# Performance work log

Measured on AMD Instinct MI355X. Metric: run time of the kernel, lower is better.

Reference implementation:

```python
import jax, jax.numpy as jnp
import numpy as np

B, C, D4, K, TOPK = 2, 16, 48, 24, 2
H, W = 512, 960
H4, W4 = H // 4, W // 4


def setup_inputs() -> dict:
    key = jax.random.key(0)
    ks = jax.random.split(key, 5)
    return {
        "att_weights": jax.random.normal(ks[0], (B, 1, D4, H4, W4), jnp.float32),
        "feat_l": jax.random.normal(ks[1], (B, C, H4, W4), jnp.float32),
        "feat_r": jax.random.normal(ks[2], (B, C, H4, W4), jnp.float32),
        "w_red": jax.random.normal(ks[3], (2 * C,), jnp.float32) / np.sqrt(2 * C).astype(np.float32),
        "spx_logits": jax.random.normal(ks[4], (B, 9, H, W), jnp.float32),
    }


def _unfold3x3(x):
    # x: [B,1,h,w] -> [B,9,h,w]; 3x3 zero-padded neighborhoods, row-major (torch F.unfold order)
    b, _, h, w = x.shape
    xp = jnp.pad(x, ((0, 0), (0, 0), (1, 1), (1, 1)))
    return jnp.concatenate([xp[:, :, dy:dy + h, dx:dx + w] for dy in range(3) for dx in range(3)], axis=1)


def _context_upsample(disp_low, spx_prob):
    # disp_low: [B,1,h,w]; spx_prob: [B,9,4h,4w] (already softmaxed over the 9 dim)
    neigh = _unfold3x3(disp_low)                                   # [B,9,h,w]
    neigh = jnp.repeat(jnp.repeat(neigh, 4, axis=2), 4, axis=3)
    return jnp.sum(neigh * spx_prob, axis=1)                        # [B,4h,4w]


def reference(att_weights, feat_l, feat_r, w_red, spx_logits):
    # ---- coarse top-K disparity selection: softmax -> sort -> gather ----
    prob = jax.nn.softmax(att_weights, axis=2)                      # [B,1,D,h,w]
    prob_t = jnp.moveaxis(prob, 2, -1)                              # [B,1,h,w,D]
    _, idx = jax.lax.top_k(prob_t, K)                               # descending by prob
    ind_k = jnp.sort(idx, axis=-1)                                  # ascending disparity order [B,1,h,w,K]
    att_topk = jnp.take_along_axis(prob_t, ind_k, axis=-1)          # [B,1,h,w,K]
    raw_t = jnp.moveaxis(att_weights, 2, -1)
    att_raw_topk = jnp.take_along_axis(raw_t, ind_k, axis=-1)       # [B,1,h,w,K]
    disp_samples = ind_k[:, 0].astype(att_weights.dtype)            # [B,h,w,K]

    att_prob = jax.nn.softmax(att_raw_topk[:, 0], axis=-1)          # [B,h,w,K]
    pred_att_x4 = jnp.sum(att_prob * disp_samples, axis=-1)         # [B,h,w]

    # ---- sparse concat volume at the K sampled disparities ----
    dK = jnp.moveaxis(ind_k[:, 0], -1, 1)                           # [B,K,h,w] int
    src = jnp.arange(W4)[None, None, None, :] - dK                  # x - d, [B,K,h,w]
    valid = (src >= 0).astype(feat_r.dtype)
    srcc = jnp.clip(src, 0, W4 - 1)
    warped_r = jnp.take_along_axis(feat_r[:, :, None, :, :], srcc[:, None], axis=-1)  # [B,C,K,h,w]
    warped_r = warped_r * valid[:, None]
    left_b = jnp.broadcast_to(feat_l[:, :, None], (feat_l.shape[0], C, K, H4, W4))
    vol = jnp.concatenate([left_b, warped_r], axis=1)               # [B,2C,K,h,w]
    vol = vol * jnp.moveaxis(att_topk, -1, 2)                       # att-weighted sparse volume

    # channel reduction -> 1-channel cost (stand-in for cat aggregation/hourglass)
    cost = jnp.einsum('bckhw,c->bkhw', vol, w_red)                  # [B,K,h,w]

    cost_t = jnp.moveaxis(cost, 1, -1)                              # [B,h,w,K]
    vals, ind2 = jax.lax.top_k(cost_t, TOPK)
    p = jax.nn.softmax(vals, axis=-1)
    dsel = jnp.take_along_axis(disp_samples, ind2, axis=-1)
    pred_x4 = jnp.sum(p * dsel, axis=-1)                            # [B,h,w]

    spx_prob = jax.nn.softmax(spx_logits, axis=1)                   # [B,9,H,W]
    pred_att_x1 = _context_upsample(pred_att_x4[:, None], spx_prob) * 4.0
    pred_x1 = _context_upsample(pred_x4[:, None], spx_prob) * 4.0
    return pred_att_x4, pred_att_x1, pred_x4, pred_x1
```

## Files before the change

### kernel.cpp

```cpp
#include <hip/hip_runtime.h>
#include <hip/hip_bf16.h>
#include <math.h>

#define Bc 2
#define Cc 16
#define D4c 48
#define Kc 24
#define Hc 512
#define Wc 960
#define H4c 128
#define W4c 240
#define HW4 (H4c * W4c)
#define S4 (Bc * HW4)
#define HW1 (Hc * Wc)
#define S1 (Bc * HW1)
#define Gg 8
#define DPT 6

__global__ __launch_bounds__(256) void k_featred(const float* __restrict__ fl,
                          const float* __restrict__ fr,
                          const float* __restrict__ wred,
                          float* __restrict__ Lred, float* __restrict__ Rred) {
    int t = blockIdx.x * blockDim.x + threadIdx.x;
    if (t >= S4 / 4) return;
    int p4 = t * 4;
    int b  = p4 / HW4;
    int hw = p4 - b * HW4;
    const float* flb = fl + (size_t)b * Cc * HW4 + hw;
    const float* frb = fr + (size_t)b * Cc * HW4 + hw;
    float4 ls = {0.f, 0.f, 0.f, 0.f}, rs = {0.f, 0.f, 0.f, 0.f};
#pragma unroll
    for (int c = 0; c < Cc; ++c) {
        float wl = wred[c], wr = wred[Cc + c];
        float4 l = *(const float4*)(flb + (size_t)c * HW4);
        float4 r = *(const float4*)(frb + (size_t)c * HW4);
        ls.x = fmaf(wl, l.x, ls.x); ls.y = fmaf(wl, l.y, ls.y);
        ls.z = fmaf(wl, l.z, ls.z); ls.w = fmaf(wl, l.w, ls.w);
        rs.x = fmaf(wr, r.x, rs.x); rs.y = fmaf(wr, r.y, rs.y);
        rs.z = fmaf(wr, r.z, rs.z); rs.w = fmaf(wr, r.w, rs.w);
    }
    *(float4*)(Lred + p4) = ls;
    *(float4*)(Rred + p4) = rs;
}

__global__ __launch_bounds__(256, 6) void k_topk(const float* __restrict__ att,
                       const float* __restrict__ Lred, const float* __restrict__ Rred,
                       float* __restrict__ oA4, float* __restrict__ oD4) {
    const int tid  = threadIdx.x;
    const int wv   = tid >> 6;
    const int lane = tid & 63;
    const int q    = lane >> 3;
    const int p    = lane & 7;
    const int pix  = blockIdx.x * 32 + wv * 8 + p;
    const int b    = pix / HW4;
    const int hw   = pix - b * HW4;
    const int col  = hw % W4c;
    const int dbase = q * DPT;

    const float* ap = att + ((size_t)b * D4c + dbase) * HW4 + hw;
    float a[DPT], RR[DPT];
#pragma unroll
    for (int i = 0; i < DPT; ++i) a[i] = ap[(size_t)i * HW4];
#pragma unroll
    for (int i = 0; i < DPT; ++i) {
        int d = dbase + i;
        RR[i] = Rred[(col >= d) ? (pix - d) : pix];
    }
    const float L = Lred[pix];

    unsigned u[DPT];
#pragma unroll
    for (int i = 0; i < DPT; ++i) {
        unsigned r = __float_as_uint(a[i]);
        u[i] = ((int)r < 0) ? ~r : (r | 0x80000000u);
    }

    float m = a[0];
#pragma unroll
    for (int i = 1; i < DPT; ++i) m = fmaxf(m, a[i]);
    m = fmaxf(m, __shfl_xor(m, 8));
    m = fmaxf(m, __shfl_xor(m, 16));
    m = fmaxf(m, __shfl_xor(m, 32));

    int bc[DPT];
#pragma unroll
    for (int i = 0; i < DPT; ++i) bc[i] = 0;
#pragma unroll
    for (int i = 0; i < DPT; ++i) {
#pragma unroll
        for (int j = i + 1; j < DPT; ++j) {
            int c = (u[i] >= u[j]) ? 1 : 0;
            bc[j] += c;
            bc[i] += 1 - c;
        }
    }
#pragma unroll 2
    for (int c = 1; c < Gg; ++c) {
        const unsigned adj = ((q ^ c) < q) ? 1u : 0u;
        unsigned ui2[DPT], uj[DPT];
#pragma unroll
        for (int i = 0; i < DPT; ++i) ui2[i] = u[i] - adj;
#pragma unroll
        for (int j = 0; j < DPT; ++j) uj[j] = __shfl_xor(u[j], c << 3);
#pragma unroll
        for (int i = 0; i < DPT; ++i) {
#pragma unroll
            for (int j = 0; j < DPT; ++j) bc[i] += (uj[j] > ui2[i]) ? 1 : 0;
        }
    }

    const float NEG = -3.0e38f;
    float s = 0.f, s2 = 0.f, n2 = 0.f;
    float v1 = NEG, v2 = NEG;
    int   i1 = 0,   i2v = 0;
#pragma unroll
    for (int i = 0; i < DPT; ++i) {
        const int d = dbase + i;
        float e = __expf(a[i] - m);
        s += e;
        bool sel = bc[i] < Kc;
        float es = sel ? e : 0.f;
        s2 += es;
        n2 = fmaf(es, (float)d, n2);
        float R = (col >= d) ? RR[i] : 0.f;
        float cst = sel ? e * (L + R) : NEG;
        bool g1 = cst > v1;
        bool g2 = cst > v2;
        float nv2 = g1 ? v1 : (g2 ? cst : v2);
        int   ni2 = g1 ? i1 : (g2 ? d : i2v);
        v1 = g1 ? cst : v1;
        i1 = g1 ? d : i1;
        v2 = nv2;
        i2v = ni2;
    }

#pragma unroll
    for (int st = 8; st <= 32; st <<= 1) {
        s  += __shfl_xor(s,  st);
        s2 += __shfl_xor(s2, st);
        n2 += __shfl_xor(n2, st);
        float ov1 = __shfl_xor(v1, st); int oi1 = __shfl_xor(i1,  st);
        float ov2 = __shfl_xor(v2, st); int oi2 = __shfl_xor(i2v, st);
        bool bt = (ov1 > v1) || (ov1 == v1 && oi1 < i1);
        float w1 = bt ? ov1 : v1;   int wi1 = bt ? oi1 : i1;
        float l1 = bt ? v1  : ov1;  int li1 = bt ? i1  : oi1;
        float w2 = bt ? ov2 : v2;   int wi2 = bt ? oi2 : i2v;
        bool b2 = (l1 > w2) || (l1 == w2 && li1 < wi2);
        v1 = w1; i1 = wi1;
        v2 = b2 ? l1 : w2;
        i2v = b2 ? li1 : wi2;
    }

    const float r = __expf((v2 - v1) / s);
    if (q == 0) {
        oA4[pix] = n2 / s2;
        oD4[pix] = ((float)i1 + r * (float)i2v) / (1.f + r);
    }
}

__global__ __launch_bounds__(256) void k_upsample(const float* __restrict__ spx,
                           const float* __restrict__ A4, const float* __restrict__ D4p,
                           float* __restrict__ oA1, float* __restrict__ oD1) {
    int t = blockIdx.x * blockDim.x + threadIdx.x;
    if (t >= S1 / 4) return;
    const int Wq  = Wc / 4;
    int xg  = t % Wq;
    int rem = t / Wq;
    int y   = rem % Hc;
    int b   = rem / Hc;
    int yx0 = y * Wc + xg * 4;

    const float* sp = spx + (size_t)b * 9 * HW1 + yx0;
    float4 e[9];
    float4 ssum = {0.f, 0.f, 0.f, 0.f};
#pragma unroll
    for (int j = 0; j < 9; ++j) {
        float4 v = *(const float4*)(sp + (size_t)j * HW1);
        e[j].x = __expf(v.x); e[j].y = __expf(v.y);
        e[j].z = __expf(v.z); e[j].w = __expf(v.w);
        ssum.x += e[j].x; ssum.y += e[j].y; ssum.z += e[j].z; ssum.w += e[j].w;
    }

    const int y4 = y >> 2, x4 = xg;
    const float* A4b = A4 + b * HW4;
    const float* D4b = D4p + b * HW4;
    float4 accA = {0.f, 0.f, 0.f, 0.f}, accD = {0.f, 0.f, 0.f, 0.f};
#pragma unroll
    for (int dy = 0; dy < 3; ++dy) {
        int yy = y4 + dy - 1;
#pragma unroll
        for (int dx = 0; dx < 3; ++dx) {
            int xx = x4 + dx - 1;
            int j = dy * 3 + dx;
            bool ok = (yy >= 0 && yy < H4c && xx >= 0 && xx < W4c);
            int pI = ok ? (yy * W4c + xx) : 0;
            float ca = ok ? A4b[pI] : 0.f;
            float cd = ok ? D4b[pI] : 0.f;
            accA.x = fmaf(e[j].x, ca, accA.x); accA.y = fmaf(e[j].y, ca, accA.y);
            accA.z = fmaf(e[j].z, ca, accA.z); accA.w = fmaf(e[j].w, ca, accA.w);
            accD.x = fmaf(e[j].x, cd, accD.x); accD.y = fmaf(e[j].y, cd, accD.y);
            accD.z = fmaf(e[j].z, cd, accD.z); accD.w = fmaf(e[j].w, cd, accD.w);
        }
    }
    float4 inv;
    inv.x = 4.f / ssum.x; inv.y = 4.f / ssum.y;
    inv.z = 4.f / ssum.z; inv.w = 4.f / ssum.w;
    float4 oA, oD;
    oA.x = accA.x * inv.x; oA.y = accA.y * inv.y;
    oA.z = accA.z * inv.z; oA.w = accA.w * inv.w;
    oD.x = accD.x * inv.x; oD.y = accD.y * inv.y;
    oD.z = accD.z * inv.z; oD.w = accD.w * inv.w;
    *(float4*)(oA1 + (size_t)b * HW1 + yx0) = oA;
    *(float4*)(oD1 + (size_t)b * HW1 + yx0) = oD;
}

extern "C" void kernel_launch(void* const* d_in, const int* in_sizes, int n_in,
                              void* d_out, int out_size, void* d_ws, size_t ws_size,
                              hipStream_t stream) {
    const float* att  = (const float*)d_in[0];
    const float* fl   = (const float*)d_in[1];
    const float* fr   = (const float*)d_in[2];
    const float* wred = (const float*)d_in[3];
    const float* spx  = (const float*)d_in[4];

    float* out = (float*)d_out;
    float* oA4 = out;
    float* oA1 = out + S4;
    float* oD4 = out + S4 + S1;
    float* oD1 = out + 2 * S4 + S1;

    float *Lred, *Rred;
    if (ws_size >= (size_t)2 * S4 * sizeof(float)) {
        Lred = (float*)d_ws;
        Rred = Lred + S4;
    } else {
        Lred = oA1;
        Rred = oA1 + S4;
    }

    k_featred<<<(S4 / 4 + 255) / 256, 256, 0, stream>>>(fl, fr, wred, Lred, Rred);
    k_topk<<<S4 / 32, 256, 0, stream>>>(att, Lred, Rred, oA4, oD4);
    k_upsample<<<(S1 / 4 + 255) / 256, 256, 0, stream>>>(spx, oA4, oD4, oA1, oD1);
}
```

Before: 33.48 us.

## Fuse feature channel reduction into top-k kernel with shared-memory halo

Removes the separate feature-reduction kernel and computes the left/right weighted channel sums inside the top-k kernel, staging a row segment plus a 47-pixel disparity halo in shared memory. This eliminates one launch and the intermediate workspace write/read. In exchange, right features are recomputed redundantly for halo pixels, and a block barrier is added. The upsample kernel also replaces division with a hardware reciprocal.

```diff
diff --git a/kernel.cpp b/kernel.cpp
--- a/kernel.cpp
+++ b/kernel.cpp
@@ -16,57 +16,66 @@
 #define S1 (Bc * HW1)
 #define Gg 8
 #define DPT 6
-
-__global__ __launch_bounds__(256) void k_featred(const float* __restrict__ fl,
-                          const float* __restrict__ fr,
-                          const float* __restrict__ wred,
-                          float* __restrict__ Lred, float* __restrict__ Rred) {
-    int t = blockIdx.x * blockDim.x + threadIdx.x;
-    if (t >= S4 / 4) return;
-    int p4 = t * 4;
-    int b  = p4 / HW4;
-    int hw = p4 - b * HW4;
-    const float* flb = fl + (size_t)b * Cc * HW4 + hw;
-    const float* frb = fr + (size_t)b * Cc * HW4 + hw;
-    float4 ls = {0.f, 0.f, 0.f, 0.f}, rs = {0.f, 0.f, 0.f, 0.f};
-#pragma unroll
-    for (int c = 0; c < Cc; ++c) {
-        float wl = wred[c], wr = wred[Cc + c];
-        float4 l = *(const float4*)(flb + (size_t)c * HW4);
-        float4 r = *(const float4*)(frb + (size_t)c * HW4);
-        ls.x = fmaf(wl, l.x, ls.x); ls.y = fmaf(wl, l.y, ls.y);
-        ls.z = fmaf(wl, l.z, ls.z); ls.w = fmaf(wl, l.w, ls.w);
-        rs.x = fmaf(wr, r.x, rs.x); rs.y = fmaf(wr, r.y, rs.y);
-        rs.z = fmaf(wr, r.z, rs.z); rs.w = fmaf(wr, r.w, rs.w);
-    }
-    *(float4*)(Lred + p4) = ls;
-    *(float4*)(Rred + p4) = rs;
-}
+#define PPB 32
+#define HALO 47
+#define RW (PPB + HALO)
 
 __global__ __launch_bounds__(256, 6) void k_topk(const float* __restrict__ att,
-                       const float* __restrict__ Lred, const float* __restrict__ Rred,
+                       const float* __restrict__ fl, const float* __restrict__ fr,
+                       const float* __restrict__ wred,
                        float* __restrict__ oA4, float* __restrict__ oD4) {
-    const int tid  = threadIdx.x;
-    const int wv   = tid >> 6;
-    const int lane = tid & 63;
-    const int q    = lane >> 3;
-    const int p    = lane & 7;
-    const int pix  = blockIdx.x * 32 + wv * 8 + p;
-    const int b    = pix / HW4;
-    const int hw   = pix - b * HW4;
-    const int col  = hw % W4c;
+    __shared__ float rrow[RW];
+    __shared__ float lrow[PPB];
+
+    const int tid   = threadIdx.x;
+    const int wv    = tid >> 6;
+    const int lane  = tid & 63;
+    const int q     = lane >> 3;
+    const int p     = lane & 7;
+    const int plocal = wv * 8 + p;
+    const int pix0  = blockIdx.x * PPB;
+    const int pix   = pix0 + plocal;
+    const int b     = pix0 / HW4;
+    const int hw    = pix - b * HW4;
+    const int col   = hw % W4c;
     const int dbase = q * DPT;
 
     const float* ap = att + ((size_t)b * D4c + dbase) * HW4 + hw;
-    float a[DPT], RR[DPT];
+    float a[DPT];
 #pragma unroll
     for (int i = 0; i < DPT; ++i) a[i] = ap[(size_t)i * HW4];
+
+    {
+        const int base = b * HW4;
+        if (tid < RW) {
+            int lin = pix0 - HALO + tid;
+            if (lin < base) lin = base;
+            const float* frb = fr + (size_t)b * Cc * HW4 + (lin - base);
+            float acc = 0.f;
+#pragma unroll
+            for (int c = 0; c < Cc; ++c)
+                acc = fmaf(wred[Cc + c], frb[(size_t)c * HW4], acc);
+            rrow[tid] = acc;
+        } else if (tid < RW + PPB) {
+            int j = tid - RW;
+            const float* flb = fl + (size_t)b * Cc * HW4 + (pix0 + j - base);
+            float acc = 0.f;
+#pragma unroll
+            for (int c = 0; c < Cc; ++c)
+                acc = fmaf(wred[c], flb[(size_t)c * HW4], acc);
+            lrow[j] = acc;
+        }
+    }
+    __syncthreads();
+
+    const float L = lrow[plocal];
+    float RR[DPT];
 #pragma unroll
     for (int i = 0; i < DPT; ++i) {
         int d = dbase + i;
-        RR[i] = Rred[(col >= d) ? (pix - d) : pix];
-    }
-    const float L = Lred[pix];
+        int idx = HALO + plocal - d;
+        RR[i] = rrow[(col >= d) ? idx : HALO + plocal];
+    }
 
     unsigned u[DPT];
 #pragma unroll
@@ -203,8 +212,10 @@
         }
     }
     float4 inv;
-    inv.x = 4.f / ssum.x; inv.y = 4.f / ssum.y;
-    inv.z = 4.f / ssum.z; inv.w = 4.f / ssum.w;
+    inv.x = 4.f * __builtin_amdgcn_rcpf(ssum.x);
+    inv.y = 4.f * __builtin_amdgcn_rcpf(ssum.y);
+    inv.z = 4.f * __builtin_amdgcn_rcpf(ssum.z);
+    inv.w = 4.f * __builtin_amdgcn_rcpf(ssum.w);
     float4 oA, oD;
     oA.x = accA.x * inv.x; oA.y = accA.y * inv.y;
     oA.z = accA.z * inv.z; oA.w = accA.w * inv.w;
@@ -229,16 +240,6 @@
     float* oD4 = out + S4 + S1;
     float* oD1 = out + 2 * S4 + S1;
 
-    float *Lred, *Rred;
-    if (ws_size >= (size_t)2 * S4 * sizeof(float)) {
-        Lred = (float*)d_ws;
-        Rred = Lred + S4;
-    } else {
-        Lred = oA1;
-        Rred = oA1 + S4;
-    }
-
-    k_featred<<<(S4 / 4 + 255) / 256, 256, 0, stream>>>(fl, fr, wred, Lred, Rred);
-    k_topk<<<S4 / 32, 256, 0, stream>>>(att, Lred, Rred, oA4, oD4);
+    k_topk<<<S4 / PPB, 256, 0, stream>>>(att, fl, fr, wred, oA4, oD4);
     k_upsample<<<(S1 / 4 + 255) / 256, 256, 0, stream>>>(spx, oA4, oD4, oA1, oD1);
 }
```

Result: faster. 31.43 us (-6.1%).
